# Kernel tuning notes

Hardware: AMD Instinct MI355X
Metric: run time of the kernel (lower is better)

Reference implementation:

```python
import jax, jax.numpy as jnp
import numpy as np

DIM = 1024
NUM_HEADS = 16
HEAD_DIM = DIM // NUM_HEADS
SCALE = HEAD_DIM ** -0.5


def setup_inputs() -> dict:
    key = jax.random.key(0)
    ks = jax.random.split(key, 5)
    x = jax.random.normal(ks[0], (4, 1024, DIM), dtype=jnp.float32)
    w_qkv = jax.random.normal(ks[1], (DIM, 3 * DIM), dtype=jnp.float32) * (DIM ** -0.5)
    b_qkv = jnp.zeros((3 * DIM,), dtype=jnp.float32)
    w_proj = jax.random.normal(ks[2], (DIM, DIM), dtype=jnp.float32) * (DIM ** -0.5)
    b_proj = jnp.zeros((DIM,), dtype=jnp.float32)
    return {"x": x, "w_qkv": w_qkv, "b_qkv": b_qkv, "w_proj": w_proj, "b_proj": b_proj}


def reference(x, w_qkv, b_qkv, w_proj, b_proj):
    B, N, C = x.shape
    qkv = x @ w_qkv + b_qkv                                  # [B, N, 3C]
    qkv = qkv.reshape(B, N, 3, NUM_HEADS, HEAD_DIM)
    qkv = jnp.transpose(qkv, (2, 0, 3, 1, 4))                # [3, B, H, N, d]
    q, k, v = qkv[0] * SCALE, qkv[1], qkv[2]
    # attn scores in float32 (clamp to finfo range is a no-op after the cast)
    attn = jnp.einsum('bhnd,bhmd->bhnm', q, k).astype(jnp.float32)
    f32 = jnp.finfo(jnp.float32)
    attn = jnp.clip(attn, f32.min, f32.max)
    attn = jax.nn.softmax(attn, axis=-1)
    out = jnp.einsum('bhnm,bhmd->bhnd', attn, v)             # [B, H, N, d]
    out = jnp.transpose(out, (0, 2, 1, 3)).reshape(B, N, C)
    return out @ w_proj + b_proj
```

## Files before the change

### kernel.cpp

```cpp
#include <hip/hip_runtime.h>


typedef _Float16 half8 __attribute__((ext_vector_type(8)));
typedef _Float16 half4v __attribute__((ext_vector_type(4)));
typedef __fp16 fp16x2 __attribute__((ext_vector_type(2)));
typedef float floatx4 __attribute__((ext_vector_type(4)));

#define MFMA16(a, b, c) __builtin_amdgcn_mfma_f32_16x16x32_f16((a), (b), (c), 0, 0, 0)

static constexpr int DIM = 1024;
static constexpr int BATCH = 4;
static constexpr int SEQ = 1024;
static constexpr int NH = 16;
static constexpr int HD = 64;
static constexpr float SCALE = 0.125f;

__device__ static inline void gld16(_Float16* lds, const _Float16* g) {
    __builtin_amdgcn_global_load_lds(
        (const __attribute__((address_space(1))) void*)g,
        (__attribute__((address_space(3))) void*)lds, 16, 0, 0);
}

__global__ __launch_bounds__(256) void prep(const float* __restrict__ x,
                                            _Float16* __restrict__ xh,
                                            const float* __restrict__ wqkv,
                                            _Float16* __restrict__ wqkvT,
                                            const float* __restrict__ wproj,
                                            _Float16* __restrict__ wprojT) {
    __shared__ float tile[32][33];
    const int bid = blockIdx.x;
    const int tid = threadIdx.x;
    if (bid < 4096) {
        int i = (bid * 256 + tid) * 4;
        float4 v = *reinterpret_cast<const float4*>(x + i);
        half4v h;
        h[0] = (_Float16)v.x; h[1] = (_Float16)v.y;
        h[2] = (_Float16)v.z; h[3] = (_Float16)v.w;
        const int m = i >> 10, k = i & 1023;
        *reinterpret_cast<half4v*>(
            &xh[((size_t)(k >> 5) * 4096 + m) * 32 + (k & 31)]) = h;
        return;
    }
    const float* in;
    _Float16* out;
    int C, NN, bx, by;
    if (bid < 7168) {
        int b = bid - 4096;
        in = wqkv; out = wqkvT; C = 3072; NN = 3072;
        bx = b % 96; by = b / 96;
    } else {
        int b = bid - 7168;
        in = wproj; out = wprojT; C = 1024; NN = 1024;
        bx = b & 31; by = b >> 5;
    }
    const int c0 = bx * 32, r0 = by * 32;
    const int tx = tid & 31, ty = tid >> 5;
#pragma unroll
    for (int j = 0; j < 32; j += 8)
        tile[ty + j][tx] = in[(size_t)(r0 + ty + j) * C + (c0 + tx)];
    __syncthreads();
#pragma unroll
    for (int j = 0; j < 32; j += 8)
        out[((size_t)(r0 >> 5) * NN + (c0 + ty + j)) * 32 + tx] =
            (_Float16)tile[tx][ty + j];
}

__global__ __launch_bounds__(512, 2) void gemm_qkv(const _Float16* __restrict__ A,
                                                   const _Float16* __restrict__ Bt,
                                                   const float* __restrict__ bias,
                                                   _Float16* __restrict__ qbuf,
                                                   _Float16* __restrict__ kbuf,
                                                   _Float16* __restrict__ vtbuf) {
    __shared__ __align__(16) _Float16 S[4][14336];

    const int tid = threadIdx.x;
    const int wid = tid >> 6;
    const int lane = tid & 63;
    const int g = lane >> 4;
    const int ln = lane & 15;
    const int wr = wid >> 1, wc = wid & 1;
    const int m0 = blockIdx.y * 256;
    const int n0 = blockIdx.x * 192;
    const bool wlt4 = wid < 4;
    const size_t PA = (size_t)4096 * 32;
    const size_t PB = (size_t)3072 * 32;
    const int lsw = (lane >> 2) * 32 + (((lane & 3) ^ ((lane >> 3) & 3)) * 8);
    const int gsw = (g ^ ((ln >> 1) & 3)) * 8;
    const _Float16* ga0 = A + (size_t)(m0 + wid * 16) * 32 + lsw;
    const _Float16* ga1 = A + (size_t)(m0 + (wid + 8) * 16) * 32 + lsw;
    const _Float16* gb0 = Bt + (size_t)(n0 + wid * 16) * 32 + lsw;
    const _Float16* gb1 = Bt + (size_t)(n0 + (wid + 8) * 16) * 32 + lsw;

    floatx4 acc[4][6];
#pragma unroll
    for (int i = 0; i < 4; ++i)
#pragma unroll
        for (int j = 0; j < 6; ++j) acc[i][j] = (floatx4){0.f, 0.f, 0.f, 0.f};

#define STAGE_A(t)                                                      \
    do {                                                                \
        gld16(&S[(t) & 3][wid * 512], ga0 + (size_t)(t) * PA);          \
        gld16(&S[(t) & 3][(wid + 8) * 512], ga1 + (size_t)(t) * PA);    \
    } while (0)
#define STAGE_B(t)                                                      \
    do {                                                                \
        gld16(&S[(t) & 3][8192 + wid * 512], gb0 + (size_t)(t) * PB);   \
        if (wlt4)                                                       \
            gld16(&S[(t) & 3][8192 + (wid + 8) * 512],                  \
                  gb1 + (size_t)(t) * PB);                              \
    } while (0)

    STAGE_A(0); STAGE_B(0);
    STAGE_A(1); STAGE_B(1);
    STAGE_A(2); STAGE_B(2);

#define COMPUTE_HALF(Sc, hh)                                                   \
    do {                                                                       \
        half8 af[2];                                                           \
        _Pragma("unroll") for (int i = 0; i < 2; ++i) af[i] =                  \
            *reinterpret_cast<const half8*>(                                   \
                &(Sc)[(wr * 64 + (hh) * 32 + i * 16 + ln) * 32 + gsw]);        \
        __builtin_amdgcn_s_setprio(1);                                         \
        _Pragma("unroll") for (int i = 0; i < 2; ++i)                          \
            _Pragma("unroll") for (int j = 0; j < 6; ++j)                      \
                acc[(hh) * 2 + i][j] = MFMA16(af[i], bf[j], acc[(hh) * 2 + i][j]); \
        __builtin_amdgcn_s_setprio(0);                                         \
    } while (0)

#define QKV_STEP(t, DO_STAGE, G4, G3)                                          \
    do {                                                                       \
        if (wlt4) asm volatile("s_waitcnt vmcnt(" G4 ")" ::: "memory");        \
        else      asm volatile("s_waitcnt vmcnt(" G3 ")" ::: "memory");        \
        __builtin_amdgcn_s_barrier();                                          \
        const _Float16* Sc = &S[(t) & 3][0];                                   \
        if (DO_STAGE) STAGE_A((t) + 3);                                        \
        half8 bf[6];                                                           \
        _Pragma("unroll") for (int j = 0; j < 6; ++j) bf[j] =                  \
            *reinterpret_cast<const half8*>(                                   \
                &Sc[8192 + (wc * 96 + j * 16 + ln) * 32 + gsw]);               \
        COMPUTE_HALF(Sc, 0);                                                   \
        if (DO_STAGE) STAGE_B((t) + 3);                                        \
        COMPUTE_HALF(Sc, 1);                                                   \
    } while (0)

    for (int t = 0; t < 29; ++t) QKV_STEP(t, true, "8", "6");
    QKV_STEP(29, false, "8", "6");
    QKV_STEP(30, false, "4", "3");
    QKV_STEP(31, false, "0", "0");

#undef QKV_STEP
#undef COMPUTE_HALF
#undef STAGE_A
#undef STAGE_B

#pragma unroll
    for (int i = 0; i < 4; ++i) {
#pragma unroll
        for (int j = 0; j < 6; ++j) {
            const int n = n0 + wc * 96 + j * 16 + ln;
            const float bn = bias[n];
            const int mrow = m0 + wr * 64 + i * 16 + g * 4;
            const int which = n >> 10;
            const int rem = n & 1023;
            const int h = rem >> 6;
            const int dd = rem & 63;
            const int b = mrow >> 10, tok = mrow & 1023;
            const int bh = b * NH + h;
            if (which == 2) {
                half4v pk;
#pragma unroll
                for (int r = 0; r < 4; ++r) pk[r] = (_Float16)(acc[i][j][r] + bn);
                *reinterpret_cast<half4v*>(
                    &vtbuf[((size_t)(bh * 32 + (tok >> 5)) * 64 + dd) * 32 +
                           (tok & 31)]) = pk;
            } else if (which == 1) {
#pragma unroll
                for (int r = 0; r < 4; ++r)
                    kbuf[((size_t)(bh * 2 + (dd >> 5)) * SEQ + tok + r) * 32 +
                         (dd & 31)] = (_Float16)(acc[i][j][r] + bn);
            } else {
#pragma unroll
                for (int r = 0; r < 4; ++r)
                    qbuf[(size_t)((bh << 10) + tok + r) * HD + dd] =
                        (_Float16)((acc[i][j][r] + bn) * SCALE);
            }
        }
    }
}

__global__ __launch_bounds__(512, 2) void gemm_proj(const _Float16* __restrict__ A,
                                                    const _Float16* __restrict__ Bt,
                                                    const float* __restrict__ bias,
                                                    float* __restrict__ outF) {
    __shared__ __align__(16) _Float16 S[4][8192];

    const int tid = threadIdx.x;
    const int wid = tid >> 6;
    const int lane = tid & 63;
    const int g = lane >> 4;
    const int ln = lane & 15;
    const int wr = wid >> 1, wc = wid & 1;
    const int m0 = blockIdx.y * 128;
    const int n0 = blockIdx.x * 128;
    const size_t PA = (size_t)4096 * 32;
    const size_t PB = (size_t)1024 * 32;
    const int lsw = (lane >> 2) * 32 + (((lane & 3) ^ ((lane >> 3) & 3)) * 8);
    const int gsw = (g ^ ((ln >> 1) & 3)) * 8;
    const _Float16* ga = A + (size_t)(m0 + wid * 16) * 32 + lsw;
    const _Float16* gb = Bt + (size_t)(n0 + wid * 16) * 32 + lsw;

    floatx4 acc[2][4];
#pragma unroll
    for (int i = 0; i < 2; ++i)
#pragma unroll
        for (int j = 0; j < 4; ++j) acc[i][j] = (floatx4){0.f, 0.f, 0.f, 0.f};

#define STAGE_A(t) gld16(&S[(t) & 3][wid * 512], ga + (size_t)(t) * PA)
#define STAGE_B(t) gld16(&S[(t) & 3][4096 + wid * 512], gb + (size_t)(t) * PB)

    STAGE_A(0); STAGE_B(0);
    STAGE_A(1); STAGE_B(1);
    STAGE_A(2); STAGE_B(2);

#define COMPUTE_HALF(Sc, hh)                                                   \
    do {                                                                       \
        half8 af = *reinterpret_cast<const half8*>(                            \
            &(Sc)[(wr * 32 + (hh) * 16 + ln) * 32 + gsw]);                     \
        __builtin_amdgcn_s_setprio(1);                                         \
        _Pragma("unroll") for (int j = 0; j < 4; ++j)                          \
            acc[hh][j] = MFMA16(af, bf[j], acc[hh][j]);                        \
        __builtin_amdgcn_s_setprio(0);                                         \
    } while (0)

#define PROJ_STEP(t, DO_STAGE, GN)                                             \
    do {                                                                       \
        asm volatile("s_waitcnt vmcnt(" GN ")" ::: "memory");                  \
        __builtin_amdgcn_s_barrier();                                          \
        const _Float16* Sc = &S[(t) & 3][0];                                   \
        if (DO_STAGE) STAGE_A((t) + 3);                                        \
        half8 bf[4];                                                           \
        _Pragma("unroll") for (int j = 0; j < 4; ++j) bf[j] =                  \
            *reinterpret_cast<const half8*>(                                   \
                &Sc[4096 + (wc * 64 + j * 16 + ln) * 32 + gsw]);               \
        COMPUTE_HALF(Sc, 0);                                                   \
        if (DO_STAGE) STAGE_B((t) + 3);                                        \
        COMPUTE_HALF(Sc, 1);                                                   \
    } while (0)

    for (int t = 0; t < 29; ++t) PROJ_STEP(t, true, "4");
    PROJ_STEP(29, false, "4");
    PROJ_STEP(30, false, "2");
    PROJ_STEP(31, false, "0");

#undef PROJ_STEP
#undef COMPUTE_HALF
#undef STAGE_A
#undef STAGE_B

#pragma unroll
    for (int i = 0; i < 2; ++i) {
#pragma unroll
        for (int j = 0; j < 4; ++j) {
            const int n = n0 + wc * 64 + j * 16 + ln;
            const float bn = bias[n];
            const int mrow = m0 + wr * 32 + i * 16 + g * 4;
#pragma unroll
            for (int r = 0; r < 4; ++r)
                outF[(size_t)(mrow + r) * 1024 + n] = acc[i][j][r] + bn;
        }
    }
}

__global__ __launch_bounds__(256, 2) void flash_attn(const _Float16* __restrict__ qbuf,
                                                     const _Float16* __restrict__ kbuf,
                                                     const _Float16* __restrict__ vtbuf,
                                                     _Float16* __restrict__ attn_out) {
    __shared__ _Float16 Klds[2 * 4096];
    __shared__ _Float16 Vlds[2 * 4096];

    const int tid = threadIdx.x;
    const int wid = tid >> 6;
    const int lane = tid & 63;
    const int g = lane >> 4;
    const int ln = lane & 15;
    const int bh = blockIdx.x;
    const int qbase = blockIdx.y * 128 + wid * 32;
    const _Float16* qg = qbuf + ((size_t)bh << 10) * HD;
    const _Float16* kg = kbuf + (size_t)bh * (2 * SEQ * 32);
    const _Float16* vg = vtbuf + (size_t)bh * (32 * 64 * 32);

    const int woff = wid * 512;
    const int lsw = (lane >> 2) * 32 + (((lane & 3) ^ ((lane >> 3) & 3)) * 8);
    const int gsw = (g ^ ((ln >> 1) & 3)) * 8;
    const int sl0 = ((lane >> 4) & 1) * 32 + ln;
    const bool hi32 = (lane & 32) != 0;

    half8 qfA[2], qfB[2];
#pragma unroll
    for (int f = 0; f < 2; ++f) {
        qfA[f] = *reinterpret_cast<const half8*>(
            qg + (size_t)(qbase + ln) * HD + f * 32 + g * 8);
        qfB[f] = *reinterpret_cast<const half8*>(
            qg + (size_t)(qbase + 16 + ln) * HD + f * 32 + g * 8);
    }

    floatx4 oA[4], oB[4];
#pragma unroll
    for (int t = 0; t < 4; ++t) {
        oA[t] = (floatx4){0.f, 0.f, 0.f, 0.f};
        oB[t] = (floatx4){0.f, 0.f, 0.f, 0.f};
    }
    float lA = 0.f, lB = 0.f;

    constexpr int NT = SEQ / 64;
#pragma unroll
    for (int f = 0; f < 2; ++f) {
        gld16(&Klds[f * 2048 + woff], kg + (size_t)f * (SEQ * 32) + woff + lsw);
        gld16(&Vlds[f * 2048 + woff], vg + (size_t)f * 2048 + woff + lsw);
    }

    for (int kt = 0; kt < NT; ++kt) {
        asm volatile("s_waitcnt vmcnt(0)" ::: "memory");
        asm volatile("s_barrier" ::: "memory");
        const int cur = kt & 1;
        if (kt < NT - 1) {
            const int nb = cur ^ 1;
#pragma unroll
            for (int f = 0; f < 2; ++f) {
                gld16(&Klds[nb * 4096 + f * 2048 + woff],
                      kg + (size_t)f * (SEQ * 32) + (kt + 1) * 2048 + woff + lsw);
                gld16(&Vlds[nb * 4096 + f * 2048 + woff],
                      vg + (size_t)(2 * (kt + 1) + f) * 2048 + woff + lsw);
            }
        }
        const _Float16* Kb = &Klds[cur * 4096];
        const _Float16* Vb = &Vlds[cur * 4096];

        half8 kf[4][2], vf[4][2];
#pragma unroll
        for (int c = 0; c < 4; ++c)
#pragma unroll
            for (int f = 0; f < 2; ++f) {
                kf[c][f] = *reinterpret_cast<const half8*>(
                    &Kb[f * 2048 + (c * 16 + ln) * 32 + gsw]);
                vf[c][f] = *reinterpret_cast<const half8*>(
                    &Vb[f * 2048 + (c * 16 + ln) * 32 + gsw]);
            }

        int pkA[4][2], pkB[4][2];
#pragma unroll
        for (int c = 0; c < 4; ++c) {
            floatx4 z = (floatx4){0.f, 0.f, 0.f, 0.f};
            z = MFMA16(kf[c][0], qfA[0], z);
            z = MFMA16(kf[c][1], qfA[1], z);
            float p0 = __expf(z[0]);
            float p1 = __expf(z[1]);
            float p2 = __expf(z[2]);
            float p3 = __expf(z[3]);
            lA += (p0 + p1) + (p2 + p3);
            union { fp16x2 h; int i; } u0, u1;
            u0.h = __builtin_amdgcn_cvt_pkrtz(p0, p1);
            u1.h = __builtin_amdgcn_cvt_pkrtz(p2, p3);
            pkA[c][0] = u0.i;
            pkA[c][1] = u1.i;
        }
#pragma unroll
        for (int c = 0; c < 4; ++c) {
            floatx4 z = (floatx4){0.f, 0.f, 0.f, 0.f};
            z = MFMA16(kf[c][0], qfB[0], z);
            z = MFMA16(kf[c][1], qfB[1], z);
            float p0 = __expf(z[0]);
            float p1 = __expf(z[1]);
            float p2 = __expf(z[2]);
            float p3 = __expf(z[3]);
            lB += (p0 + p1) + (p2 + p3);
            union { fp16x2 h; int i; } u0, u1;
            u0.h = __builtin_amdgcn_cvt_pkrtz(p0, p1);
            u1.h = __builtin_amdgcn_cvt_pkrtz(p2, p3);
            pkB[c][0] = u0.i;
            pkB[c][1] = u1.i;
        }

#pragma unroll
        for (int H = 0; H < 2; ++H) {
            {
                int a0 = __shfl(pkA[2 * H][0], sl0), b0 = __shfl(pkA[2 * H + 1][0], sl0);
                int a1 = __shfl(pkA[2 * H][1], sl0), b1 = __shfl(pkA[2 * H + 1][1], sl0);
                int a2 = __shfl(pkA[2 * H][0], sl0 + 16), b2 = __shfl(pkA[2 * H + 1][0], sl0 + 16);
                int a3 = __shfl(pkA[2 * H][1], sl0 + 16), b3 = __shfl(pkA[2 * H + 1][1], sl0 + 16);
                union { int i[4]; half8 h; } ua;
                ua.i[0] = hi32 ? b0 : a0;
                ua.i[1] = hi32 ? b1 : a1;
                ua.i[2] = hi32 ? b2 : a2;
                ua.i[3] = hi32 ? b3 : a3;
#pragma unroll
                for (int t = 0; t < 4; ++t) oA[t] = MFMA16(ua.h, vf[t][H], oA[t]);
            }
            {
                int a0 = __shfl(pkB[2 * H][0], sl0), b0 = __shfl(pkB[2 * H + 1][0], sl0);
                int a1 = __shfl(pkB[2 * H][1], sl0), b1 = __shfl(pkB[2 * H + 1][1], sl0);
                int a2 = __shfl(pkB[2 * H][0], sl0 + 16), b2 = __shfl(pkB[2 * H + 1][0], sl0 + 16);
                int a3 = __shfl(pkB[2 * H][1], sl0 + 16), b3 = __shfl(pkB[2 * H + 1][1], sl0 + 16);
                union { int i[4]; half8 h; } ua;
                ua.i[0] = hi32 ? b0 : a0;
                ua.i[1] = hi32 ? b1 : a1;
                ua.i[2] = hi32 ? b2 : a2;
                ua.i[3] = hi32 ? b3 : a3;
#pragma unroll
                for (int t = 0; t < 4; ++t) oB[t] = MFMA16(ua.h, vf[t][H], oB[t]);
            }
        }
    }

    lA += __shfl_xor(lA, 16);
    lA += __shfl_xor(lA, 32);
    lB += __shfl_xor(lB, 16);
    lB += __shfl_xor(lB, 32);

    const int b = bh >> 4, h = bh & 15;
#pragma unroll
    for (int r = 0; r < 4; ++r) {
        const float invA = 1.0f / __shfl(lA, g * 4 + r);
        const float invB = 1.0f / __shfl(lB, g * 4 + r);
        const int tokA = qbase + g * 4 + r;
        const int tokB = tokA + 16;
#pragma unroll
        for (int t = 0; t < 4; ++t) {
            attn_out[((size_t)(h * 2 + (t >> 1)) * 4096 + (b * SEQ + tokA)) * 32 +
                     (t & 1) * 16 + ln] = (_Float16)(oA[t][r] * invA);
            attn_out[((size_t)(h * 2 + (t >> 1)) * 4096 + (b * SEQ + tokB)) * 32 +
                     (t & 1) * 16 + ln] = (_Float16)(oB[t][r] * invB);
        }
    }
}

extern "C" void kernel_launch(void* const* d_in, const int* in_sizes, int n_in,
                              void* d_out, int out_size, void* d_ws, size_t ws_size,
                              hipStream_t stream) {
    const float* x = (const float*)d_in[0];
    const float* wqkv = (const float*)d_in[1];
    const float* bqkv = (const float*)d_in[2];
    const float* wproj = (const float*)d_in[3];
    const float* bproj = (const float*)d_in[4];
    float* out = (float*)d_out;

    char* ws = (char*)d_ws;
    _Float16* xh     = (_Float16*)(ws);
    _Float16* wqkvT  = (_Float16*)(ws + (8ull << 20));
    _Float16* qbuf   = (_Float16*)(ws + (14ull << 20));
    _Float16* kbuf   = (_Float16*)(ws + (22ull << 20));
    _Float16* vtbuf  = (_Float16*)(ws + (30ull << 20));
    _Float16* wprojT = (_Float16*)(ws + (38ull << 20));
    _Float16* attn   = xh;

    prep<<<8192, 256, 0, stream>>>(x, xh, wqkv, wqkvT, wproj, wprojT);
    gemm_qkv<<<dim3(16, 16), 512, 0, stream>>>(xh, wqkvT, bqkv, qbuf, kbuf, vtbuf);
    flash_attn<<<dim3(BATCH * NH, SEQ / 128), 256, 0, stream>>>(qbuf, kbuf, vtbuf, attn);
    gemm_proj<<<dim3(8, 32), 512, 0, stream>>>(attn, wprojT, bproj, out);
}
```

Baseline: 162.6 us.

## Use 4 waves per block in QKV GEMM with doubled per-wave M tile

The QKV GEMM block drops from 512 to 256 threads while keeping the same 256x192 block tile. Each wave now computes 128x96 outputs (8x6 MFMA accumulators) and issues 4 A and 3 B global-to-LDS loads per stage, with the vmcnt waits adjusted to match. This doubles reuse of the B fragments loaded from LDS and removes the uneven wave split for B staging. The cost is about twice the accumulator registers per wave and half as many waves for hiding latency, which may lower occupancy or cause spills.

```diff
diff --git a/kernel.cpp b/kernel.cpp
--- a/kernel.cpp
+++ b/kernel.cpp
@@ -65,7 +65,7 @@
             (_Float16)tile[tx][ty + j];
 }
 
-__global__ __launch_bounds__(512, 2) void gemm_qkv(const _Float16* __restrict__ A,
+__global__ __launch_bounds__(256, 2) void gemm_qkv(const _Float16* __restrict__ A,
                                                    const _Float16* __restrict__ Bt,
                                                    const float* __restrict__ bias,
                                                    _Float16* __restrict__ qbuf,
@@ -81,33 +81,30 @@
     const int wr = wid >> 1, wc = wid & 1;
     const int m0 = blockIdx.y * 256;
     const int n0 = blockIdx.x * 192;
-    const bool wlt4 = wid < 4;
     const size_t PA = (size_t)4096 * 32;
     const size_t PB = (size_t)3072 * 32;
     const int lsw = (lane >> 2) * 32 + (((lane & 3) ^ ((lane >> 3) & 3)) * 8);
     const int gsw = (g ^ ((ln >> 1) & 3)) * 8;
-    const _Float16* ga0 = A + (size_t)(m0 + wid * 16) * 32 + lsw;
-    const _Float16* ga1 = A + (size_t)(m0 + (wid + 8) * 16) * 32 + lsw;
-    const _Float16* gb0 = Bt + (size_t)(n0 + wid * 16) * 32 + lsw;
-    const _Float16* gb1 = Bt + (size_t)(n0 + (wid + 8) * 16) * 32 + lsw;
-
-    floatx4 acc[4][6];
-#pragma unroll
-    for (int i = 0; i < 4; ++i)
+    const _Float16* ga = A + (size_t)(m0 + wid * 16) * 32 + lsw;
+    const _Float16* gb = Bt + (size_t)(n0 + wid * 16) * 32 + lsw;
+
+    floatx4 acc[8][6];
+#pragma unroll
+    for (int i = 0; i < 8; ++i)
 #pragma unroll
         for (int j = 0; j < 6; ++j) acc[i][j] = (floatx4){0.f, 0.f, 0.f, 0.f};
 
-#define STAGE_A(t)                                                      \
-    do {                                                                \
-        gld16(&S[(t) & 3][wid * 512], ga0 + (size_t)(t) * PA);          \
-        gld16(&S[(t) & 3][(wid + 8) * 512], ga1 + (size_t)(t) * PA);    \
-    } while (0)
-#define STAGE_B(t)                                                      \
-    do {                                                                \
-        gld16(&S[(t) & 3][8192 + wid * 512], gb0 + (size_t)(t) * PB);   \
-        if (wlt4)                                                       \
-            gld16(&S[(t) & 3][8192 + (wid + 8) * 512],                  \
-                  gb1 + (size_t)(t) * PB);                              \
+#define STAGE_A(t)                                                            \
+    do {                                                                      \
+        _Pragma("unroll") for (int c = 0; c < 4; ++c)                         \
+            gld16(&S[(t) & 3][(wid + 4 * c) * 512],                           \
+                  ga + (size_t)(4 * c * 16) * 32 + (size_t)(t) * PA);         \
+    } while (0)
+#define STAGE_B(t)                                                            \
+    do {                                                                      \
+        _Pragma("unroll") for (int c = 0; c < 3; ++c)                         \
+            gld16(&S[(t) & 3][8192 + (wid + 4 * c) * 512],                    \
+                  gb + (size_t)(4 * c * 16) * 32 + (size_t)(t) * PB);         \
     } while (0)
 
     STAGE_A(0); STAGE_B(0);
@@ -116,21 +113,20 @@
 
 #define COMPUTE_HALF(Sc, hh)                                                   \
     do {                                                                       \
-        half8 af[2];                                                           \
-        _Pragma("unroll") for (int i = 0; i < 2; ++i) af[i] =                  \
+        half8 af[4];                                                           \
+        _Pragma("unroll") for (int i = 0; i < 4; ++i) af[i] =                  \
             *reinterpret_cast<const half8*>(                                   \
-                &(Sc)[(wr * 64 + (hh) * 32 + i * 16 + ln) * 32 + gsw]);        \
+                &(Sc)[(wr * 128 + (hh) * 64 + i * 16 + ln) * 32 + gsw]);       \
         __builtin_amdgcn_s_setprio(1);                                         \
-        _Pragma("unroll") for (int i = 0; i < 2; ++i)                          \
+        _Pragma("unroll") for (int i = 0; i < 4; ++i)                          \
             _Pragma("unroll") for (int j = 0; j < 6; ++j)                      \
-                acc[(hh) * 2 + i][j] = MFMA16(af[i], bf[j], acc[(hh) * 2 + i][j]); \
+                acc[(hh) * 4 + i][j] = MFMA16(af[i], bf[j], acc[(hh) * 4 + i][j]); \
         __builtin_amdgcn_s_setprio(0);                                         \
     } while (0)
 
-#define QKV_STEP(t, DO_STAGE, G4, G3)                                          \
+#define QKV_STEP(t, DO_STAGE, GN)                                              \
     do {                                                                       \
-        if (wlt4) asm volatile("s_waitcnt vmcnt(" G4 ")" ::: "memory");        \
-        else      asm volatile("s_waitcnt vmcnt(" G3 ")" ::: "memory");        \
+        asm volatile("s_waitcnt vmcnt(" GN ")" ::: "memory");                  \
         __builtin_amdgcn_s_barrier();                                          \
         const _Float16* Sc = &S[(t) & 3][0];                                   \
         if (DO_STAGE) STAGE_A((t) + 3);                                        \
@@ -143,10 +139,10 @@
         COMPUTE_HALF(Sc, 1);                                                   \
     } while (0)
 
-    for (int t = 0; t < 29; ++t) QKV_STEP(t, true, "8", "6");
-    QKV_STEP(29, false, "8", "6");
-    QKV_STEP(30, false, "4", "3");
-    QKV_STEP(31, false, "0", "0");
+    for (int t = 0; t < 29; ++t) QKV_STEP(t, true, "14");
+    QKV_STEP(29, false, "14");
+    QKV_STEP(30, false, "7");
+    QKV_STEP(31, false, "0");
 
 #undef QKV_STEP
 #undef COMPUTE_HALF
@@ -154,12 +150,12 @@
 #undef STAGE_B
 
 #pragma unroll
-    for (int i = 0; i < 4; ++i) {
+    for (int i = 0; i < 8; ++i) {
 #pragma unroll
         for (int j = 0; j < 6; ++j) {
             const int n = n0 + wc * 96 + j * 16 + ln;
             const float bn = bias[n];
-            const int mrow = m0 + wr * 64 + i * 16 + g * 4;
+            const int mrow = m0 + wr * 128 + i * 16 + g * 4;
             const int which = n >> 10;
             const int rem = n & 1023;
             const int h = rem >> 6;
@@ -454,7 +450,7 @@
     _Float16* attn   = xh;
 
     prep<<<8192, 256, 0, stream>>>(x, xh, wqkv, wqkvT, wproj, wprojT);
-    gemm_qkv<<<dim3(16, 16), 512, 0, stream>>>(xh, wqkvT, bqkv, qbuf, kbuf, vtbuf);
+    gemm_qkv<<<dim3(16, 16), 256, 0, stream>>>(xh, wqkvT, bqkv, qbuf, kbuf, vtbuf);
     flash_attn<<<dim3(BATCH * NH, SEQ / 128), 256, 0, stream>>>(qbuf, kbuf, vtbuf, attn);
     gemm_proj<<<dim3(8, 32), 512, 0, stream>>>(attn, wprojT, bproj, out);
 }
```

New measurement: 170.7 us. 5.0% more time.
